# Optimization experiments

Measured on AMD Instinct MI355X. Metric: run time of the kernel, lower is better.

Reference implementation:

```python
import jax, jax.numpy as jnp
import numpy as np

D_MODEL = 1024
N_HEAD = 16
D_HEAD = D_MODEL // N_HEAD
EXP = 4
B, T = 2, 2048
EPS = 1e-5

def setup_inputs() -> dict:
    key = jax.random.key(0)
    ks = jax.random.split(key, 16)
    s = 0.02
    return {
        "x": jax.random.normal(ks[0], (B, T, D_MODEL), jnp.float32),
        "ln1_w": jnp.ones((D_MODEL,), jnp.float32),
        "ln1_b": jnp.zeros((D_MODEL,), jnp.float32),
        "attn_w": jax.random.normal(ks[1], (D_MODEL, 3 * D_MODEL), jnp.float32) * s,
        "attn_b": jnp.zeros((3 * D_MODEL,), jnp.float32),
        "proj_w": jax.random.normal(ks[2], (D_MODEL, D_MODEL), jnp.float32) * s,
        "proj_b": jnp.zeros((D_MODEL,), jnp.float32),
        "ln2_w": jnp.ones((D_MODEL,), jnp.float32),
        "ln2_b": jnp.zeros((D_MODEL,), jnp.float32),
        "fc_w": jax.random.normal(ks[3], (D_MODEL, EXP * D_MODEL), jnp.float32) * s,
        "fc_b": jnp.zeros((EXP * D_MODEL,), jnp.float32),
        "fc2_w": jax.random.normal(ks[4], (EXP * D_MODEL, D_MODEL), jnp.float32) * s,
        "fc2_b": jnp.zeros((D_MODEL,), jnp.float32),
    }

def _layernorm(x, w, b):
    mu = jnp.mean(x, axis=-1, keepdims=True)
    var = jnp.mean(jnp.square(x - mu), axis=-1, keepdims=True)
    return (x - mu) * jax.lax.rsqrt(var + EPS) * w + b

def _attn(x, attn_w, attn_b, proj_w, proj_b):
    Bx, Tx, C = x.shape
    qkv = x @ attn_w + attn_b  # [B,T,3C]
    q, k, v = jnp.split(qkv, 3, axis=-1)
    # [B, H, T, Dh]
    q = q.reshape(Bx, Tx, N_HEAD, D_HEAD).transpose(0, 2, 1, 3)
    k = k.reshape(Bx, Tx, N_HEAD, D_HEAD).transpose(0, 2, 1, 3)
    v = v.reshape(Bx, Tx, N_HEAD, D_HEAD).transpose(0, 2, 1, 3)
    att = jnp.einsum('bhqd,bhkd->bhqk', q, k) * (1.0 / np.sqrt(D_HEAD))
    causal = jnp.tril(jnp.ones((Tx, Tx), bool))
    att = jnp.where(causal, att, -jnp.inf)
    att = jax.nn.softmax(att, axis=-1)
    y = jnp.einsum('bhqk,bhkd->bhqd', att, v)
    y = y.transpose(0, 2, 1, 3).reshape(Bx, Tx, C)
    return y @ proj_w + proj_b

def reference(x, ln1_w, ln1_b, attn_w, attn_b, proj_w, proj_b,
              ln2_w, ln2_b, fc_w, fc_b, fc2_w, fc2_b):
    x = x + _attn(_layernorm(x, ln1_w, ln1_b), attn_w, attn_b, proj_w, proj_b)
    h = _layernorm(x, ln2_w, ln2_b)
    h = jax.nn.gelu(h @ fc_w + fc_b, approximate=False)  # exact GELU (torch nn.GELU default)
    x = x + (h @ fc2_w + fc2_b)
    return x
```

## Files before the change

kernel.cpp:

```cpp
#include <hip/hip_runtime.h>
#include <hip/hip_bf16.h>
#include <math.h>


#define D_MODEL 1024
#define N_HEAD  16
#define D_HEAD  64
#define SEQ_T   2048
#define BATCH   2
#define NROWS   (BATCH * SEQ_T)
#define C3      (3 * D_MODEL)
#define D_FF    (4 * D_MODEL)

typedef __bf16 bf16x8 __attribute__((ext_vector_type(8)));
typedef __bf16 bf16x4t __attribute__((ext_vector_type(4)));
typedef short  s16x4  __attribute__((ext_vector_type(4)));
typedef float  f32x4  __attribute__((ext_vector_type(4)));

#define WAIT_VM8() asm volatile("s_waitcnt vmcnt(8)" ::: "memory")

__device__ __forceinline__ f32x4 mfma16_bf16(s16x4 a, s16x4 b, f32x4 c)
{
#if __has_builtin(__builtin_amdgcn_mfma_f32_16x16x16_bf16)
    return __builtin_amdgcn_mfma_f32_16x16x16_bf16(
        __builtin_bit_cast(bf16x4t, a), __builtin_bit_cast(bf16x4t, b), c, 0, 0, 0);
#else
    return __builtin_amdgcn_mfma_f32_16x16x16bf16_1k(a, b, c, 0, 0, 0);
#endif
}

__global__ __launch_bounds__(256) void ln_kernel(
    const float* __restrict__ in, const float* __restrict__ w,
    const float* __restrict__ b, __hip_bfloat16* __restrict__ out, int D)
{
    const int row = blockIdx.x;
    const int tid = threadIdx.x;
    const float* x = in + (size_t)row * D;

    float s = 0.f, s2 = 0.f;
    for (int i = tid; i < D; i += 256) {
        float v = x[i];
        s += v; s2 += v * v;
    }
    __shared__ float rs[256], rs2[256];
    rs[tid] = s; rs2[tid] = s2;
    __syncthreads();
    for (int off = 128; off > 0; off >>= 1) {
        if (tid < off) { rs[tid] += rs[tid + off]; rs2[tid] += rs2[tid + off]; }
        __syncthreads();
    }
    const float mu   = rs[0] / D;
    const float var  = rs2[0] / D - mu * mu;
    const float rstd = rsqrtf(var + 1e-5f);

    __hip_bfloat16* o = out + (size_t)row * D;
    for (int i = tid; i < D; i += 256)
        o[i] = __float2bfloat16((x[i] - mu) * rstd * w[i] + b[i]);
}

__global__ __launch_bounds__(256) void transpose_all_kernel(
    const float* __restrict__ attn_w, const float* __restrict__ proj_w,
    const float* __restrict__ fc_w,   const float* __restrict__ fc2_w,
    __hip_bfloat16* __restrict__ attn_wt, __hip_bfloat16* __restrict__ proj_wt,
    __hip_bfloat16* __restrict__ fc_wt,   __hip_bfloat16* __restrict__ fc2_wt)
{
    __shared__ float t[32][33];
    int tb = blockIdx.x;
    const float* W; __hip_bfloat16* Wt; int K, N;
    if (tb < 3072)      { W = attn_w; Wt = attn_wt; K = D_MODEL; N = C3; }
    else if (tb < 4096) { tb -= 3072; W = proj_w; Wt = proj_wt; K = D_MODEL; N = D_MODEL; }
    else if (tb < 8192) { tb -= 4096; W = fc_w;   Wt = fc_wt;   K = D_MODEL; N = D_FF; }
    else                { tb -= 8192; W = fc2_w;  Wt = fc2_wt;  K = D_FF;    N = D_MODEL; }
    const int ntx = N >> 5;
    const int k0 = (tb / ntx) * 32;
    const int n0 = (tb % ntx) * 32;

    const int tx = threadIdx.x & 31;
    const int ty = threadIdx.x >> 5;
#pragma unroll
    for (int i = 0; i < 4; ++i)
        t[ty + 8 * i][tx] = W[(size_t)(k0 + ty + 8 * i) * N + n0 + tx];
    __syncthreads();
#pragma unroll
    for (int i = 0; i < 4; ++i)
        Wt[(size_t)(n0 + ty + 8 * i) * K + k0 + tx] =
            __float2bfloat16(t[tx][ty + 8 * i]);
}

__device__ __forceinline__ void async16(const __hip_bfloat16* g, __hip_bfloat16* l)
{
    __builtin_amdgcn_global_load_lds(
        (const __attribute__((address_space(1))) void*)g,
        (__attribute__((address_space(3))) void*)l, 16, 0, 0);
}

__device__ __forceinline__ float gelu_exact(float v)
{
    return 0.5f * v * (1.0f + erff(v * 0.70710678118654752f));
}

__device__ __forceinline__ void swz_xcd(int& bx, int& by)
{
    const int nbx = gridDim.x;
    const int nwg = nbx * gridDim.y;
    int lin = blockIdx.y * nbx + blockIdx.x;
    const int per = nwg >> 3;
    lin = (lin & 7) * per + (lin >> 3);
    bx = lin % nbx;
    by = lin / nbx;
}


template<int NL, int TPB>
__device__ __forceinline__ void stage_slice(
    const __hip_bfloat16* __restrict__ g, int K,
    __hip_bfloat16* __restrict__ ldst, int tid)
{
#pragma unroll
    for (int i = 0; i < NL; ++i)
        async16(g + (size_t)(i * (TPB / 4)) * K, ldst + i * (TPB / 4) * 32 + tid * 8);
}

__device__ __forceinline__ void gemm_rot4_512(
    const __hip_bfloat16* __restrict__ A,
    const __hip_bfloat16* __restrict__ Bt,
    int K, int row0, int col0, f32x4 (&acc)[8][4])
{
    __shared__ __align__(16) __hip_bfloat16 Asl[4][256 * 32];
    __shared__ __align__(16) __hip_bfloat16 Bsl[4][256 * 32];

    const int tid  = threadIdx.x;
    const int wv   = tid >> 6;
    const int lane = tid & 63;
    const int ln15 = lane & 15;
    const int lq   = lane >> 4;
    const int mbase = (wv >> 2) * 128;
    const int nbase = (wv & 3) * 64;
    const int rcol = (lq ^ ((ln15 >> 1) & 3)) * 8;
    const int ssw  = ((tid & 3) ^ ((tid >> 3) & 3)) * 8;
    const __hip_bfloat16* Ab = A  + (size_t)(row0 + (tid >> 2)) * K + ssw;
    const __hip_bfloat16* Bb = Bt + (size_t)(col0 + (tid >> 2)) * K + ssw;
    const int nt = K >> 5;

#pragma unroll
    for (int mi = 0; mi < 8; ++mi)
#pragma unroll
        for (int ni = 0; ni < 4; ++ni) acc[mi][ni] = (f32x4){0.f, 0.f, 0.f, 0.f};

#pragma unroll
    for (int t = 0; t < 3; ++t) {
        stage_slice<2, 512>(Ab + t * 32, K, &Asl[t][0], tid);
        stage_slice<2, 512>(Bb + t * 32, K, &Bsl[t][0], tid);
    }
    WAIT_VM8();
    __builtin_amdgcn_s_barrier();

    for (int tq = 0; tq < nt; tq += 4) {
#pragma unroll
        for (int u = 0; u < 4; ++u) {
            const int t   = tq + u;
            const int tcl = (t + 3 < nt) ? t + 3 : nt - 1;
            const int sl  = u;
            const int sl3 = (u + 3) & 3;
            bf16x8 af[4], bfr[4];

#pragma unroll
            for (int mi = 0; mi < 4; ++mi)
                af[mi] = *(const bf16x8*)&Asl[sl][(mbase + mi * 16 + ln15) * 32 + rcol];
#pragma unroll
            for (int ni = 0; ni < 4; ++ni)
                bfr[ni] = *(const bf16x8*)&Bsl[sl][(nbase + ni * 16 + ln15) * 32 + rcol];
            stage_slice<2, 512>(Ab + (size_t)tcl * 32, K, &Asl[sl3][0], tid);
            __builtin_amdgcn_s_barrier();
            __builtin_amdgcn_s_setprio(1);
#pragma unroll
            for (int mi = 0; mi < 4; ++mi)
#pragma unroll
                for (int ni = 0; ni < 4; ++ni)
                    acc[mi][ni] = __builtin_amdgcn_mfma_f32_16x16x32_bf16(
                        af[mi], bfr[ni], acc[mi][ni], 0, 0, 0);
            __builtin_amdgcn_s_setprio(0);
            __builtin_amdgcn_s_barrier();

#pragma unroll
            for (int mi = 0; mi < 4; ++mi)
                af[mi] = *(const bf16x8*)&Asl[sl][(mbase + 64 + mi * 16 + ln15) * 32 + rcol];
            stage_slice<2, 512>(Bb + (size_t)tcl * 32, K, &Bsl[sl3][0], tid);
            WAIT_VM8();
            __builtin_amdgcn_s_barrier();
            __builtin_amdgcn_s_setprio(1);
#pragma unroll
            for (int mi = 0; mi < 4; ++mi)
#pragma unroll
                for (int ni = 0; ni < 4; ++ni)
                    acc[4 + mi][ni] = __builtin_amdgcn_mfma_f32_16x16x32_bf16(
                        af[mi], bfr[ni], acc[4 + mi][ni], 0, 0, 0);
            __builtin_amdgcn_s_setprio(0);
            __builtin_amdgcn_s_barrier();
        }
    }
}

__device__ __forceinline__ void gemm_rot4_256(
    const __hip_bfloat16* __restrict__ A,
    const __hip_bfloat16* __restrict__ Bt,
    int K, int row0, int col0, f32x4 (&acc)[4][4])
{
    __shared__ __align__(16) __hip_bfloat16 Asl[4][128 * 32];
    __shared__ __align__(16) __hip_bfloat16 Bsl[4][128 * 32];

    const int tid  = threadIdx.x;
    const int wv   = tid >> 6;
    const int lane = tid & 63;
    const int ln15 = lane & 15;
    const int lq   = lane >> 4;
    const int mbase = (wv >> 1) * 64;
    const int nbase = (wv & 1) * 64;
    const int rcol = (lq ^ ((ln15 >> 1) & 3)) * 8;
    const int ssw  = ((tid & 3) ^ ((tid >> 3) & 3)) * 8;
    const __hip_bfloat16* Ab = A  + (size_t)(row0 + (tid >> 2)) * K + ssw;
    const __hip_bfloat16* Bb = Bt + (size_t)(col0 + (tid >> 2)) * K + ssw;
    const int nt = K >> 5;

#pragma unroll
    for (int mi = 0; mi < 4; ++mi)
#pragma unroll
        for (int ni = 0; ni < 4; ++ni) acc[mi][ni] = (f32x4){0.f, 0.f, 0.f, 0.f};

#pragma unroll
    for (int t = 0; t < 3; ++t) {
        stage_slice<2, 256>(Ab + t * 32, K, &Asl[t][0], tid);
        stage_slice<2, 256>(Bb + t * 32, K, &Bsl[t][0], tid);
    }
    WAIT_VM8();
    __builtin_amdgcn_s_barrier();

    for (int tq = 0; tq < nt; tq += 4) {
#pragma unroll
        for (int u = 0; u < 4; ++u) {
            const int t   = tq + u;
            const int tcl = (t + 3 < nt) ? t + 3 : nt - 1;
            const int sl  = u;
            const int sl3 = (u + 3) & 3;
            bf16x8 af[4], bfr[4];

#pragma unroll
            for (int mi = 0; mi < 4; ++mi)
                af[mi] = *(const bf16x8*)&Asl[sl][(mbase + mi * 16 + ln15) * 32 + rcol];
#pragma unroll
            for (int ni = 0; ni < 4; ++ni)
                bfr[ni] = *(const bf16x8*)&Bsl[sl][(nbase + ni * 16 + ln15) * 32 + rcol];
            stage_slice<2, 256>(Ab + (size_t)tcl * 32, K, &Asl[sl3][0], tid);
            stage_slice<2, 256>(Bb + (size_t)tcl * 32, K, &Bsl[sl3][0], tid);
            WAIT_VM8();
            __builtin_amdgcn_s_barrier();
            __builtin_amdgcn_s_setprio(1);
#pragma unroll
            for (int mi = 0; mi < 4; ++mi)
#pragma unroll
                for (int ni = 0; ni < 4; ++ni)
                    acc[mi][ni] = __builtin_amdgcn_mfma_f32_16x16x32_bf16(
                        af[mi], bfr[ni], acc[mi][ni], 0, 0, 0);
            __builtin_amdgcn_s_setprio(0);
            __builtin_amdgcn_s_barrier();
        }
    }
}

__global__ __launch_bounds__(512) void gemm256_kernel(
    const __hip_bfloat16* __restrict__ A,
    const __hip_bfloat16* __restrict__ Bt,
    const float* __restrict__ bias,
    const float* __restrict__ residual,
    void* __restrict__ Cout,
    int M, int N, int K, int act, int outBf16)
{
    int bx, by;
    swz_xcd(bx, by);
    const int row0 = by * 256;
    const int col0 = bx * 256;

    f32x4 acc[8][4];
    gemm_rot4_512(A, Bt, K, row0, col0, acc);

    const int tid  = threadIdx.x;
    const int wv   = tid >> 6;
    const int lane = tid & 63;
    const int ln15 = lane & 15;
    const int lq   = lane >> 4;
    const int mbase = (wv >> 2) * 128;
    const int nbase = (wv & 3) * 64;

#pragma unroll
    for (int mi = 0; mi < 8; ++mi) {
#pragma unroll
        for (int ni = 0; ni < 4; ++ni) {
            const int gc = col0 + nbase + ni * 16 + ln15;
            const float bv = bias[gc];
#pragma unroll
            for (int r = 0; r < 4; ++r) {
                const int gr = row0 + mbase + mi * 16 + lq * 4 + r;
                float v = acc[mi][ni][r] + bv;
                if (act == 1) v = gelu_exact(v);
                if (residual) v += residual[(size_t)gr * N + gc];
                if (outBf16)
                    ((__hip_bfloat16*)Cout)[(size_t)gr * N + gc] = __float2bfloat16(v);
                else
                    ((float*)Cout)[(size_t)gr * N + gc] = v;
            }
        }
    }
}

__global__ __launch_bounds__(256, 2) void gemm128_kernel(
    const __hip_bfloat16* __restrict__ A,
    const __hip_bfloat16* __restrict__ Bt,
    const float* __restrict__ bias,
    const float* __restrict__ residual,
    void* __restrict__ Cout,
    int M, int N, int K, int act, int outBf16)
{
    int bx, by;
    swz_xcd(bx, by);
    const int row0 = by * 128;
    const int col0 = bx * 128;

    f32x4 acc[4][4];
    gemm_rot4_256(A, Bt, K, row0, col0, acc);

    const int tid  = threadIdx.x;
    const int wv   = tid >> 6;
    const int lane = tid & 63;
    const int ln15 = lane & 15;
    const int lq   = lane >> 4;
    const int mbase = (wv >> 1) * 64;
    const int nbase = (wv & 1) * 64;

#pragma unroll
    for (int mi = 0; mi < 4; ++mi) {
#pragma unroll
        for (int ni = 0; ni < 4; ++ni) {
            const int gc = col0 + nbase + ni * 16 + ln15;
            const float bv = bias[gc];
#pragma unroll
            for (int r = 0; r < 4; ++r) {
                const int gr = row0 + mbase + mi * 16 + lq * 4 + r;
                float v = acc[mi][ni][r] + bv;
                if (act == 1) v = gelu_exact(v);
                if (residual) v += residual[(size_t)gr * N + gc];
                if (outBf16)
                    ((__hip_bfloat16*)Cout)[(size_t)gr * N + gc] = __float2bfloat16(v);
                else
                    ((float*)Cout)[(size_t)gr * N + gc] = v;
            }
        }
    }
}

__global__ __launch_bounds__(512) void qkv256_kernel(
    const __hip_bfloat16* __restrict__ A,
    const __hip_bfloat16* __restrict__ Bt,
    const float* __restrict__ bias,
    __hip_bfloat16* __restrict__ Qb,
    __hip_bfloat16* __restrict__ Kb,
    __hip_bfloat16* __restrict__ Vtb)
{
    int bx, by;
    swz_xcd(bx, by);
    const int row0 = by * 256;
    const int col0 = bx * 256;

    f32x4 acc[8][4];
    gemm_rot4_512(A, Bt, D_MODEL, row0, col0, acc);

    const int tid  = threadIdx.x;
    const int wv   = tid >> 6;
    const int lane = tid & 63;
    const int ln15 = lane & 15;
    const int lq   = lane >> 4;
    const int mbase = (wv >> 2) * 128;
    const int nbase = (wv & 3) * 64;

#pragma unroll
    for (int mi = 0; mi < 8; ++mi) {
        const int gr0 = row0 + mbase + mi * 16 + lq * 4;
        const int bb  = gr0 >> 11;
        const int q0  = gr0 & 2047;
#pragma unroll
        for (int ni = 0; ni < 4; ++ni) {
            const int gc  = col0 + nbase + ni * 16 + ln15;
            const float bv = bias[gc];
            const int sec = gc >> 10;
            const int hd  = (gc & 1023) >> 6;
            const int d   = gc & 63;
            if (sec == 2) {
                unsigned short u[4];
#pragma unroll
                for (int r = 0; r < 4; ++r) {
                    __hip_bfloat16 e = __float2bfloat16(acc[mi][ni][r] + bv);
                    u[r] = *(unsigned short*)&e;
                }
                uint2 pk;
                pk.x = (unsigned int)u[0] | ((unsigned int)u[1] << 16);
                pk.y = (unsigned int)u[2] | ((unsigned int)u[3] << 16);
                *(uint2*)(Vtb + ((size_t)((bb * N_HEAD + hd) * D_HEAD + d)) * SEQ_T + q0) = pk;
            } else {
                __hip_bfloat16* dst = (sec == 0 ? Qb : Kb)
                    + ((size_t)((bb * N_HEAD + hd) * SEQ_T + q0)) * D_HEAD + d;
#pragma unroll
                for (int r = 0; r < 4; ++r)
                    dst[(size_t)r * D_HEAD] = __float2bfloat16(acc[mi][ni][r] + bv);
            }
        }
    }
}

#define ATQ 64
#define ATK 128
#define NQT (SEQ_T / ATQ)
#define KP  72
#define VP  136

__global__ __launch_bounds__(256) void mfma_attn_kernel(
    const __hip_bfloat16* __restrict__ Qb,
    const __hip_bfloat16* __restrict__ Kb,
    const __hip_bfloat16* __restrict__ Vtb,
    __hip_bfloat16* __restrict__ y)
{
    __shared__ __align__(16) __hip_bfloat16 Ks[ATK * KP];
    __shared__ __align__(16) __hip_bfloat16 Vts[D_HEAD * VP];

    const int pair = blockIdx.x;
    const int h    = blockIdx.y;
    const int b    = blockIdx.z;
    const int tid  = threadIdx.x;
    const int wv   = tid >> 6;
    const int lane = tid & 63;
    const int ln15 = lane & 15;
    const int lq   = lane >> 4;

    const __hip_bfloat16* Qh = Qb  + (size_t)(b * N_HEAD + h) * SEQ_T * D_HEAD;
    const __hip_bfloat16* Kh = Kb  + (size_t)(b * N_HEAD + h) * SEQ_T * D_HEAD;
    const __hip_bfloat16* Vh = Vtb + (size_t)(b * N_HEAD + h) * D_HEAD * SEQ_T;
    const size_t bT = (size_t)b * SEQ_T;

    const float CEXP = 0.18033688011f;

#pragma unroll 1
    for (int half = 0; half < 2; ++half) {
        const int qt    = half == 0 ? pair : (NQT - 1 - pair);
        const int qbase = qt * ATQ;
        const int ntk   = (qt >> 1) + 1;
        const int qg    = qbase + wv * 16 + ln15;

        bf16x8 qf[2];
#pragma unroll
        for (int kc = 0; kc < 2; ++kc)
            qf[kc] = *(const bf16x8*)(Qh + (size_t)(qbase + wv * 16 + ln15) * D_HEAD
                                      + kc * 32 + lq * 8);

        f32x4 Oacc[4];
#pragma unroll
        for (int dn = 0; dn < 4; ++dn) Oacc[dn] = (f32x4){0.f, 0.f, 0.f, 0.f};
        float m_run = -INFINITY, l_run = 0.f;

        for (int t = 0; t < ntk; ++t) {
            const int kb = t * ATK;
            __syncthreads();
#pragma unroll
            for (int i = 0; i < 4; ++i) {
                const int ch = tid + i * 256;
                const int r = ch >> 3, c8 = (ch & 7) * 8;
                *(bf16x8*)&Ks[r * KP + c8] =
                    *(const bf16x8*)(Kh + (size_t)(kb + r) * D_HEAD + c8);
            }
#pragma unroll
            for (int i = 0; i < 4; ++i) {
                const int ch = tid + i * 256;
                const int r = ch >> 4, c8 = (ch & 15) * 8;
                *(bf16x8*)&Vts[r * VP + c8] =
                    *(const bf16x8*)(Vh + (size_t)r * SEQ_T + kb + c8);
            }
            __syncthreads();

            f32x4 st[8];
#pragma unroll
            for (int jf = 0; jf < 8; ++jf) st[jf] = (f32x4){0.f, 0.f, 0.f, 0.f};
#pragma unroll
            for (int jf = 0; jf < 8; ++jf) {
                const bf16x8 kf0 = *(const bf16x8*)&Ks[(jf * 16 + ln15) * KP + lq * 8];
                const bf16x8 kf1 = *(const bf16x8*)&Ks[(jf * 16 + ln15) * KP + 32 + lq * 8];
                st[jf] = __builtin_amdgcn_mfma_f32_16x16x32_bf16(kf0, qf[0], st[jf], 0, 0, 0);
                st[jf] = __builtin_amdgcn_mfma_f32_16x16x32_bf16(kf1, qf[1], st[jf], 0, 0, 0);
            }

            if (t == ntk - 1) {
#pragma unroll
                for (int jf = 0; jf < 8; ++jf)
#pragma unroll
                    for (int r = 0; r < 4; ++r)
                        if ((kb + jf * 16 + lq * 4 + r) > qg) st[jf][r] = -INFINITY;
            }

            float tmax = st[0][0];
#pragma unroll
            for (int jf = 0; jf < 8; ++jf)
#pragma unroll
                for (int r = 0; r < 4; ++r) tmax = fmaxf(tmax, st[jf][r]);
            tmax = fmaxf(tmax, __shfl_xor(tmax, 16));
            tmax = fmaxf(tmax, __shfl_xor(tmax, 32));
            const float mnew  = fmaxf(m_run, tmax);
            const float alpha = exp2f((m_run - mnew) * CEXP);
            const float mc    = mnew * CEXP;
            float psum = 0.f;
#pragma unroll
            for (int jf = 0; jf < 8; ++jf)
#pragma unroll
                for (int r = 0; r < 4; ++r) {
                    const float p = exp2f(fmaf(st[jf][r], CEXP, -mc));
                    st[jf][r] = p;
                    psum += p;
                }
            psum += __shfl_xor(psum, 16);
            psum += __shfl_xor(psum, 32);
            l_run = alpha * l_run + psum;
            m_run = mnew;

            float a4[4];
#pragma unroll
            for (int r = 0; r < 4; ++r) a4[r] = __shfl(alpha, lq * 4 + r);
#pragma unroll
            for (int dn = 0; dn < 4; ++dn)
#pragma unroll
                for (int r = 0; r < 4; ++r) Oacc[dn][r] *= a4[r];

#pragma unroll
            for (int jf = 0; jf < 8; ++jf) {
                s16x4 pfr;
#pragma unroll
                for (int s = 0; s < 4; ++s) {
                    __hip_bfloat16 e = __float2bfloat16(st[jf][s]);
                    pfr[s] = __builtin_bit_cast(short, e);
                }
#pragma unroll
                for (int dn = 0; dn < 4; ++dn) {
                    const s16x4 vfr = *(const s16x4*)&Vts[(dn * 16 + ln15) * VP
                                                          + jf * 16 + lq * 4];
                    Oacc[dn] = mfma16_bf16(pfr, vfr, Oacc[dn]);
                }
            }
        }

        __syncthreads();
        float il[4];
#pragma unroll
        for (int r = 0; r < 4; ++r) il[r] = 1.0f / __shfl(l_run, lq * 4 + r);
#pragma unroll
        for (int dn = 0; dn < 4; ++dn)
#pragma unroll
            for (int r = 0; r < 4; ++r)
                Ks[(wv * 16 + lq * 4 + r) * 72 + dn * 16 + ln15] =
                    __float2bfloat16(Oacc[dn][r] * il[r]);
        const int r2 = lane >> 3, c8 = (lane & 7) * 8;
#pragma unroll
        for (int i = 0; i < 2; ++i) {
            const int row = wv * 16 + r2 + 8 * i;
            const bf16x8 val = *(const bf16x8*)&Ks[row * 72 + c8];
            *(bf16x8*)(y + (bT + qbase + row) * D_MODEL + h * D_HEAD + c8) = val;
        }
    }
}

extern "C" void kernel_launch(void* const* d_in, const int* in_sizes, int n_in,
                              void* d_out, int out_size, void* d_ws, size_t ws_size,
                              hipStream_t stream)
{
    const float* x      = (const float*)d_in[0];
    const float* ln1_w  = (const float*)d_in[1];
    const float* ln1_b  = (const float*)d_in[2];
    const float* attn_w = (const float*)d_in[3];
    const float* attn_b = (const float*)d_in[4];
    const float* proj_w = (const float*)d_in[5];
    const float* proj_b = (const float*)d_in[6];
    const float* ln2_w  = (const float*)d_in[7];
    const float* ln2_b  = (const float*)d_in[8];
    const float* fc_w   = (const float*)d_in[9];
    const float* fc_b   = (const float*)d_in[10];
    const float* fc2_w  = (const float*)d_in[11];
    const float* fc2_b  = (const float*)d_in[12];
    float* out = (float*)d_out;

    char* ws = (char*)d_ws;
    __hip_bfloat16* Qb      = (__hip_bfloat16*)(ws);
    __hip_bfloat16* Kb      = (__hip_bfloat16*)(ws + (size_t)8  * 1024 * 1024);
    __hip_bfloat16* Vtb     = (__hip_bfloat16*)(ws + (size_t)16 * 1024 * 1024);
    __hip_bfloat16* h_bf    = (__hip_bfloat16*)(ws);
    __hip_bfloat16* ln_buf  = (__hip_bfloat16*)(ws + (size_t)32 * 1024 * 1024);
    __hip_bfloat16* y_buf   = (__hip_bfloat16*)(ws + (size_t)40 * 1024 * 1024);
    float*          xmid    = (float*)(ws + (size_t)48 * 1024 * 1024);
    __hip_bfloat16* attn_wt = (__hip_bfloat16*)(ws + (size_t)64 * 1024 * 1024);
    __hip_bfloat16* proj_wt = (__hip_bfloat16*)(ws + (size_t)70 * 1024 * 1024);
    __hip_bfloat16* fc_wt   = (__hip_bfloat16*)(ws + (size_t)72 * 1024 * 1024);
    __hip_bfloat16* fc2_wt  = (__hip_bfloat16*)(ws + (size_t)80 * 1024 * 1024);

    dim3 blk256(256);
    dim3 blk512(512);

    transpose_all_kernel<<<dim3(12288), blk256, 0, stream>>>(
        attn_w, proj_w, fc_w, fc2_w, attn_wt, proj_wt, fc_wt, fc2_wt);

    ln_kernel<<<dim3(NROWS), blk256, 0, stream>>>(x, ln1_w, ln1_b, ln_buf, D_MODEL);

    qkv256_kernel<<<dim3(C3 / 256, NROWS / 256), blk512, 0, stream>>>(
        ln_buf, attn_wt, attn_b, Qb, Kb, Vtb);

    mfma_attn_kernel<<<dim3(NQT / 2, N_HEAD, BATCH), blk256, 0, stream>>>(
        Qb, Kb, Vtb, y_buf);

    gemm128_kernel<<<dim3(D_MODEL / 128, NROWS / 128), blk256, 0, stream>>>(
        y_buf, proj_wt, proj_b, x, xmid, NROWS, D_MODEL, D_MODEL, 0, 0);

    ln_kernel<<<dim3(NROWS), blk256, 0, stream>>>(xmid, ln2_w, ln2_b, ln_buf, D_MODEL);

    gemm256_kernel<<<dim3(D_FF / 256, NROWS / 256), blk512, 0, stream>>>(
        ln_buf, fc_wt, fc_b, nullptr, h_bf, NROWS, D_FF, D_MODEL, 1, 1);

    gemm128_kernel<<<dim3(D_MODEL / 128, NROWS / 128), blk256, 0, stream>>>(
        h_bf, fc2_wt, fc2_b, xmid, out, NROWS, D_MODEL, D_FF, 0, 0);
}
```

Before: 403.9 us.

## Prefetch K/V tiles via registers, swizzle LDS layout, remap blocks across XCDs

The attention kernel now loads the next K/V tile into registers while the current tile is being computed, then writes it to LDS at the start of the next iteration. This replaces the old load-then-sync pattern that exposed global-memory latency on every tile. Row padding in LDS is replaced by XOR-swizzled addressing to avoid bank conflicts without spending extra LDS. Block indices are remapped so heads are spread across the XCDs, and s_setprio raises wave priority around the MFMA loops. The cost is extra register pressure from the staging buffers and added index arithmetic.

Measured after the change: 388.6 us. 1.04x faster.

```diff
diff --git a/kernel.cpp b/kernel.cpp
--- a/kernel.cpp
+++ b/kernel.cpp
@@ -418,8 +418,6 @@
 #define ATQ 64
 #define ATK 128
 #define NQT (SEQ_T / ATQ)
-#define KP  72
-#define VP  136
 
 __global__ __launch_bounds__(256) void mfma_attn_kernel(
     const __hip_bfloat16* __restrict__ Qb,
@@ -427,12 +425,17 @@
     const __hip_bfloat16* __restrict__ Vtb,
     __hip_bfloat16* __restrict__ y)
 {
-    __shared__ __align__(16) __hip_bfloat16 Ks[ATK * KP];
-    __shared__ __align__(16) __hip_bfloat16 Vts[D_HEAD * VP];
-
-    const int pair = blockIdx.x;
-    const int h    = blockIdx.y;
-    const int b    = blockIdx.z;
+    __shared__ __align__(16) __hip_bfloat16 Ks[ATK * D_HEAD];
+    __shared__ __align__(16) __hip_bfloat16 Vts[D_HEAD * ATK];
+
+    const int flat = (blockIdx.z * gridDim.y + blockIdx.y) * gridDim.x + blockIdx.x;
+    const int xcd  = flat & 7;
+    const int slot = flat >> 3;
+    const int pair = slot & 15;
+    const int hb   = slot >> 4;
+    const int h    = xcd + 8 * (hb & 1);
+    const int b    = hb >> 1;
+
     const int tid  = threadIdx.x;
     const int wv   = tid >> 6;
     const int lane = tid & 63;
@@ -445,6 +448,32 @@
     const size_t bT = (size_t)b * SEQ_T;
 
     const float CEXP = 0.18033688011f;
+
+    bf16x8 kreg[4], vreg[4];
+    const int kr = tid >> 3, kg = tid & 7;
+    const int vr = tid >> 4, vc = tid & 15;
+
+    auto issue = [&](int kb) {
+#pragma unroll
+        for (int i = 0; i < 4; ++i)
+            kreg[i] = *(const bf16x8*)(Kh + (size_t)(kb + kr + i * 32) * D_HEAD + kg * 8);
+#pragma unroll
+        for (int i = 0; i < 4; ++i)
+            vreg[i] = *(const bf16x8*)(Vh + (size_t)(vr + i * 16) * SEQ_T + kb + vc * 8);
+    };
+    auto commit = [&]() {
+#pragma unroll
+        for (int i = 0; i < 4; ++i) {
+            const int r = kr + i * 32;
+            *(bf16x8*)&Ks[r * 64 + ((kg ^ (r & 7)) << 3)] = kreg[i];
+        }
+#pragma unroll
+        for (int i = 0; i < 4; ++i) {
+            const int r = vr + i * 16;
+            const int g8 = vc * 2;
+            *(bf16x8*)&Vts[r * 128 + ((g8 ^ ((r & 3) << 2)) << 2)] = vreg[i];
+        }
+    };
 
 #pragma unroll 1
     for (int half = 0; half < 2; ++half) {
@@ -464,35 +493,27 @@
         for (int dn = 0; dn < 4; ++dn) Oacc[dn] = (f32x4){0.f, 0.f, 0.f, 0.f};
         float m_run = -INFINITY, l_run = 0.f;
 
+        issue(0);
+
         for (int t = 0; t < ntk; ++t) {
             const int kb = t * ATK;
+            commit();
             __syncthreads();
-#pragma unroll
-            for (int i = 0; i < 4; ++i) {
-                const int ch = tid + i * 256;
-                const int r = ch >> 3, c8 = (ch & 7) * 8;
-                *(bf16x8*)&Ks[r * KP + c8] =
-                    *(const bf16x8*)(Kh + (size_t)(kb + r) * D_HEAD + c8);
-            }
-#pragma unroll
-            for (int i = 0; i < 4; ++i) {
-                const int ch = tid + i * 256;
-                const int r = ch >> 4, c8 = (ch & 15) * 8;
-                *(bf16x8*)&Vts[r * VP + c8] =
-                    *(const bf16x8*)(Vh + (size_t)r * SEQ_T + kb + c8);
-            }
-            __syncthreads();
+            if (t + 1 < ntk) issue((t + 1) * ATK);
 
             f32x4 st[8];
 #pragma unroll
             for (int jf = 0; jf < 8; ++jf) st[jf] = (f32x4){0.f, 0.f, 0.f, 0.f};
+            __builtin_amdgcn_s_setprio(1);
 #pragma unroll
             for (int jf = 0; jf < 8; ++jf) {
-                const bf16x8 kf0 = *(const bf16x8*)&Ks[(jf * 16 + ln15) * KP + lq * 8];
-                const bf16x8 kf1 = *(const bf16x8*)&Ks[(jf * 16 + ln15) * KP + 32 + lq * 8];
+                const int rw = jf * 16 + ln15;
+                const bf16x8 kf0 = *(const bf16x8*)&Ks[rw * 64 + ((lq ^ (ln15 & 7)) << 3)];
+                const bf16x8 kf1 = *(const bf16x8*)&Ks[rw * 64 + (((4 + lq) ^ (ln15 & 7)) << 3)];
                 st[jf] = __builtin_amdgcn_mfma_f32_16x16x32_bf16(kf0, qf[0], st[jf], 0, 0, 0);
                 st[jf] = __builtin_amdgcn_mfma_f32_16x16x32_bf16(kf1, qf[1], st[jf], 0, 0, 0);
             }
+            __builtin_amdgcn_s_setprio(0);
 
             if (t == ntk - 1) {
 #pragma unroll
@@ -534,6 +555,7 @@
 #pragma unroll
                 for (int r = 0; r < 4; ++r) Oacc[dn][r] *= a4[r];
 
+            __builtin_amdgcn_s_setprio(1);
 #pragma unroll
             for (int jf = 0; jf < 8; ++jf) {
                 s16x4 pfr;
@@ -544,14 +566,16 @@
                 }
 #pragma unroll
                 for (int dn = 0; dn < 4; ++dn) {
-                    const s16x4 vfr = *(const s16x4*)&Vts[(dn * 16 + ln15) * VP
-                                                          + jf * 16 + lq * 4];
+                    const int rw = dn * 16 + ln15;
+                    const int g8 = (jf * 4 + lq) ^ ((ln15 & 3) << 2);
+                    const s16x4 vfr = *(const s16x4*)&Vts[rw * 128 + (g8 << 2)];
                     Oacc[dn] = mfma16_bf16(pfr, vfr, Oacc[dn]);
                 }
             }
-        }
-
-        __syncthreads();
+            __builtin_amdgcn_s_setprio(0);
+            __syncthreads();
+        }
+
         float il[4];
 #pragma unroll
         for (int r = 0; r < 4; ++r) il[r] = 1.0f / __shfl(l_run, lq * 4 + r);
@@ -568,6 +592,7 @@
             const bf16x8 val = *(const bf16x8*)&Ks[row * 72 + c8];
             *(bf16x8*)(y + (bT + qbase + row) * D_MODEL + h * D_HEAD + c8) = val;
         }
+        __syncthreads();
     }
 }
 
```
